# Kernel optimization log

Hardware: AMD Instinct MI355X
Metric: run time of the kernel (lower is better)

The kernel has to match this reference:

```python
import jax, jax.numpy as jnp
import numpy as np

N, E, D, D_OUT = 100000, 3200000, 64, 64
EPS = 1e-5


def setup_inputs() -> dict:
    key = jax.random.key(0)
    ks = jax.random.split(key, 16)
    s = 1.0 / np.sqrt(D)
    inp = {
        "x": jax.random.normal(ks[0], (N, D), dtype=jnp.float32),
        "edge_index": jax.random.randint(ks[1], (2, E), 0, N, dtype=jnp.int64),
        # layer 1: GCNConv weight/bias, fc weight/bias, BN gamma/beta
        "W1": jax.random.uniform(ks[2], (D, D), jnp.float32, -s, s),
        "b1": jnp.zeros((D,), jnp.float32),
        "fw1": jax.random.uniform(ks[3], (D, D), jnp.float32, -s, s),
        "fb1": jax.random.uniform(ks[4], (D,), jnp.float32, -s, s),
        "g1": jnp.ones((D,), jnp.float32),
        "bt1": jnp.zeros((D,), jnp.float32),
        # layer 2
        "W2": jax.random.uniform(ks[5], (D, D), jnp.float32, -s, s),
        "b2": jnp.zeros((D,), jnp.float32),
        "fw2": jax.random.uniform(ks[6], (D, D_OUT), jnp.float32, -s, s),
        "fb2": jax.random.uniform(ks[7], (D_OUT,), jnp.float32, -s, s),
        "g2": jnp.ones((D_OUT,), jnp.float32),
        "bt2": jnp.zeros((D_OUT,), jnp.float32),
    }
    return inp


def _gcn_conv(x, W, b, src, dst, dinv):
    # x' = X W, then symmetric-normalized scatter-add aggregation (self loops included)
    h = x @ W                                   # [N, D]
    msg = (dinv[src] * dinv[dst])[:, None] * h[src]  # [E+N, D]
    out = jax.ops.segment_sum(msg, dst, num_segments=N)
    return out + b


def _fc_bn_relu(x, fw, fb, g, bt):
    y = x @ fw + fb
    mu = jnp.mean(y, axis=0)
    var = jnp.mean((y - mu) ** 2, axis=0)  # biased var (torch BN training mode)
    y = (y - mu) * jax.lax.rsqrt(var + EPS) * g + bt
    return jax.nn.relu(y)


def reference(x, edge_index, W1, b1, fw1, fb1, g1, bt1, W2, b2, fw2, fb2, g2, bt2):
    loop = jnp.arange(N, dtype=edge_index.dtype)
    src = jnp.concatenate([edge_index[0], loop])  # add self loops
    dst = jnp.concatenate([edge_index[1], loop])
    deg = jax.ops.segment_sum(jnp.ones_like(dst, dtype=x.dtype), dst, num_segments=N)
    dinv = jax.lax.rsqrt(deg)  # deg >= 1 thanks to self loops

    h = _gcn_conv(x, W1, b1, src, dst, dinv)
    h = _fc_bn_relu(h, fw1, fb1, g1, bt1)
    h = _gcn_conv(h, W2, b2, src, dst, dinv)
    h = _fc_bn_relu(h, fw2, fb2, g2, bt2)
    return h
```

## Files before the change

### kernel.cpp

```cpp
#include <hip/hip_runtime.h>

#define N_NODES 100000
#define N_EDGES 3200000
#define D 64
#define EPS 1e-5f

#define BSHIFT 7
#define BNODES 128
#define NBUCK ((N_NODES + BNODES - 1) / BNODES)
#define P1_CHUNK 8192
#define NB_P1 ((N_EDGES + P1_CHUNK - 1) / P1_CHUNK)
#define SRC_MASK 0x1FFFFu
#define BCAP 4480
#define TBL_STRIDE 784

typedef __attribute__((ext_vector_type(8))) short bf16x8;
typedef __attribute__((ext_vector_type(4))) float f32x4;

__device__ __forceinline__ unsigned short f2bf(float f) {
  unsigned int u = __float_as_uint(f);
  u += 0x7FFFu + ((u >> 16) & 1u);
  return (unsigned short)(u >> 16);
}
__device__ __forceinline__ float bf2f(unsigned short h) {
  return __uint_as_float(((unsigned int)h) << 16);
}
__device__ __forceinline__ float2 bfpair(unsigned int u) {
  return make_float2(__uint_as_float(u << 16), __uint_as_float(u & 0xFFFF0000u));
}
__device__ __forceinline__ void addp(float2 a[4], uint4 u) {
  a[0] += bfpair(u.x);
  a[1] += bfpair(u.y);
  a[2] += bfpair(u.z);
  a[3] += bfpair(u.w);
}

__global__ __launch_bounds__(256) void combine_weights(
    const float* __restrict__ W1, const float* __restrict__ b1,
    const float* __restrict__ fw1, const float* __restrict__ fb1,
    const float* __restrict__ W2, const float* __restrict__ b2,
    const float* __restrict__ fw2, const float* __restrict__ fb2,
    unsigned int* __restrict__ WcB1, float* __restrict__ bc1,
    unsigned int* __restrict__ WcB2, float* __restrict__ bc2,
    float* __restrict__ stats) {
  if (blockIdx.x == 2) {
    if (threadIdx.x < 256) stats[threadIdx.x] = 0.0f;
    return;
  }
  const float* W  = blockIdx.x ? W2  : W1;
  const float* fw = blockIdx.x ? fw2 : fw1;
  const float* b  = blockIdx.x ? b2  : b1;
  const float* fb = blockIdx.x ? fb2 : fb1;
  unsigned int* WcB = blockIdx.x ? WcB2 : WcB1;
  float* bc = blockIdx.x ? bc2 : bc1;

  __shared__ float sW[64 * 64];
  __shared__ float sf[64 * 64];
  __shared__ float sC[64 * 64];
  for (int i = threadIdx.x; i < 4096; i += 256) { sW[i] = W[i]; sf[i] = fw[i]; }
  __syncthreads();
  for (int o = threadIdx.x; o < 4096; o += 256) {
    int i = o >> 6, j = o & 63;
    float acc = 0.f;
    #pragma unroll
    for (int k = 0; k < 64; ++k) acc += sW[i * 64 + k] * sf[k * 64 + j];
    sC[o] = acc;
  }
  __syncthreads();
  for (int o = threadIdx.x; o < 2048; o += 256) {
    int jj = o & 3, L = (o >> 2) & 63, kh = (o >> 8) & 1, nt = o >> 9;
    int k0 = (L >> 4) * 8 + jj * 2 + kh * 32;
    int n  = nt * 16 + (L & 15);
    unsigned int lo = f2bf(sC[k0 * 64 + n]);
    unsigned int hi = f2bf(sC[(k0 + 1) * 64 + n]);
    WcB[o] = (hi << 16) | lo;
  }
  if (threadIdx.x < 64) {
    int j = threadIdx.x;
    float acc = fb[j];
    #pragma unroll
    for (int k = 0; k < 64; ++k) acc += b[k] * sf[k * 64 + j];
    bc[j] = acc;
  }
}

__global__ __launch_bounds__(512) void pass1_sort(
    const int* __restrict__ src, const int* __restrict__ dst,
    unsigned int* __restrict__ stage, unsigned short* __restrict__ tbl) {
  __shared__ unsigned int hist[NBUCK];
  __shared__ unsigned int ts[512];
  __shared__ unsigned int sorted[P1_CHUNK];
  const int tid = threadIdx.x;
  const int e0 = blockIdx.x * P1_CHUNK;

  for (int b = tid; b < NBUCK; b += 512) hist[b] = 0;
  __syncthreads();

  int dreg[16];
  #pragma unroll
  for (int k = 0; k < 16; ++k) {
    int e = e0 + k * 512 + tid;
    int d = (e < N_EDGES) ? dst[e] : -1;
    dreg[k] = d;
    if (d >= 0) atomicAdd(&hist[((unsigned)d) >> BSHIFT], 1u);
  }
  __syncthreads();

  unsigned int v0 = (2 * tid < NBUCK) ? hist[2 * tid] : 0u;
  unsigned int v1 = (2 * tid + 1 < NBUCK) ? hist[2 * tid + 1] : 0u;
  unsigned int run = v0 + v1;
  ts[tid] = run;
  __syncthreads();
  for (int o = 1; o < 512; o <<= 1) {
    unsigned int add = (tid >= o) ? ts[tid - o] : 0u;
    __syncthreads();
    ts[tid] += add;
    __syncthreads();
  }
  const unsigned int excl = ts[tid] - run;
  const unsigned int m = ts[511];
  unsigned short* trow = tbl + (size_t)blockIdx.x * TBL_STRIDE;
  if (2 * tid < NBUCK)     { hist[2 * tid]     = excl;      trow[2 * tid]     = (unsigned short)excl; }
  if (2 * tid + 1 < NBUCK) { hist[2 * tid + 1] = excl + v0; trow[2 * tid + 1] = (unsigned short)(excl + v0); }
  if (tid == 0) trow[NBUCK] = (unsigned short)m;
  __syncthreads();

  #pragma unroll
  for (int k = 0; k < 16; ++k) {
    int e = e0 + k * 512 + tid;
    int t = dreg[k];
    if (t >= 0) {
      unsigned int pos = atomicAdd(&hist[((unsigned)t) >> BSHIFT], 1u);
      sorted[pos] = (((unsigned)(t & (BNODES - 1))) << 17) | (unsigned)src[e];
    }
  }
  __syncthreads();

  unsigned int* so = stage + (size_t)blockIdx.x * P1_CHUNK;
  for (int i = tid; i < (int)m; i += 512) so[i] = sorted[i];
}

__global__ __launch_bounds__(512) void pass2_sort(
    const unsigned int* __restrict__ stage, const unsigned short* __restrict__ tbl,
    int* __restrict__ eSrc, int* __restrict__ off, int* __restrict__ edeg,
    float* __restrict__ dinv, const float* __restrict__ x,
    unsigned short* __restrict__ Xs) {
  __shared__ int segbase[NB_P1];
  __shared__ int spre[512];
  __shared__ int cnt[BNODES];
  __shared__ int ts[BNODES];
  __shared__ float dinvL[BNODES];
  __shared__ unsigned int raw[BCAP];
  __shared__ int sorted[BCAP];
  const int b = blockIdx.x, tid = threadIdx.x;
  const int n0 = b * BNODES;

  int len = 0;
  if (tid < NB_P1) {
    const unsigned short* trow = tbl + (size_t)tid * TBL_STRIDE;
    int o0 = trow[b], o1 = trow[b + 1];
    segbase[tid] = tid * P1_CHUNK + o0;
    len = o1 - o0;
  }
  if (tid < BNODES) cnt[tid] = 0;
  spre[tid] = len;
  __syncthreads();
  for (int o = 1; o < 512; o <<= 1) {
    int add = (tid >= o) ? spre[tid - o] : 0;
    __syncthreads();
    spre[tid] += add;
    __syncthreads();
  }
  const int m = spre[511];
  const int pref = spre[tid] - len;

  if (tid < NB_P1) {
    const int base = segbase[tid];
    for (int j = 0; j < len; ++j) {
      unsigned int p = stage[base + j];
      raw[pref + j] = p;
      atomicAdd(&cnt[p >> 17], 1);
    }
  }
  __syncthreads();

  int v = 0;
  if (tid < BNODES) { v = cnt[tid]; ts[tid] = v; }
  __syncthreads();
  for (int o = 1; o < BNODES; o <<= 1) {
    int add = (tid >= o && tid < BNODES) ? ts[tid - o] : 0;
    __syncthreads();
    if (tid < BNODES) ts[tid] += add;
    __syncthreads();
  }
  if (tid < BNODES) {
    int excl = ts[tid] - v;
    int node = n0 + tid;
    float dv = rsqrtf((float)v + 1.0f);
    dinvL[tid] = dv;
    if (node < N_NODES) {
      off[node]  = b * BCAP + excl;
      edeg[node] = v;
      dinv[node] = dv;
    }
    cnt[tid] = excl;
  }
  __syncthreads();

  for (int i = tid; i < m; i += 512) {
    unsigned int p = raw[i];
    int pos = atomicAdd(&cnt[p >> 17], 1);
    if (pos < BCAP) sorted[pos] = (int)(p & SRC_MASK);
  }
  __syncthreads();

  int* out = eSrc + (size_t)b * BCAP;
  for (int i = tid; i < m; i += 512) out[i] = sorted[i];

  const int rows = min(BNODES, N_NODES - n0);
  for (int i = tid; i < rows * 64; i += 512) {
    int r = i >> 6;
    size_t g = (size_t)(n0 + r) * 64 + (i & 63);
    Xs[g] = f2bf(dinvL[r] * x[g]);
  }
}

__global__ __launch_bounds__(256) void agg_csr(
    const int* __restrict__ off, const int* __restrict__ edeg,
    const int* __restrict__ eSrc, const unsigned short* __restrict__ Xs,
    const float* __restrict__ dinv, unsigned short* __restrict__ agg) {
  const int wid = (blockIdx.x * 256 + threadIdx.x) >> 6;
  const int lane = threadIdx.x & 63;
  const int grp = lane >> 3, sub = lane & 7;
  if (wid >= N_NODES) return;
  const int s0 = off[wid];
  const int s1 = s0 + edeg[wid];
  const uint4* XsV = (const uint4*)Xs;

  float2 acc[4];
  {
    uint4 u = XsV[(size_t)wid * 8 + sub];
    if (grp != 0) { u.x = 0; u.y = 0; u.z = 0; u.w = 0; }
    acc[0] = bfpair(u.x);
    acc[1] = bfpair(u.y);
    acc[2] = bfpair(u.z);
    acc[3] = bfpair(u.w);
  }

  int e = s0;
  const int eend = s1 - ((s1 - s0) & 31);
  for (; e < eend; e += 32) {
    int sa = eSrc[e + grp];
    int sb = eSrc[e + 8 + grp];
    int sc = eSrc[e + 16 + grp];
    int sd = eSrc[e + 24 + grp];
    uint4 ua = XsV[(size_t)sa * 8 + sub];
    uint4 ub = XsV[(size_t)sb * 8 + sub];
    uint4 uc = XsV[(size_t)sc * 8 + sub];
    uint4 ud = XsV[(size_t)sd * 8 + sub];
    addp(acc, ua); addp(acc, ub); addp(acc, uc); addp(acc, ud);
  }
  if (e < s1) {
    const int lim = s1 - 1;
    int ea = e + grp, eb = e + 8 + grp, ec = e + 16 + grp, ed = e + 24 + grp;
    int sa = eSrc[min(ea, lim)];
    int sb = eSrc[min(eb, lim)];
    int sc = eSrc[min(ec, lim)];
    int sd = eSrc[min(ed, lim)];
    uint4 ua = XsV[(size_t)sa * 8 + sub];
    uint4 ub = XsV[(size_t)sb * 8 + sub];
    uint4 uc = XsV[(size_t)sc * 8 + sub];
    uint4 ud = XsV[(size_t)sd * 8 + sub];
    if (ea > lim) { ua.x = 0; ua.y = 0; ua.z = 0; ua.w = 0; }
    if (eb > lim) { ub.x = 0; ub.y = 0; ub.z = 0; ub.w = 0; }
    if (ec > lim) { uc.x = 0; uc.y = 0; uc.z = 0; uc.w = 0; }
    if (ed > lim) { ud.x = 0; ud.y = 0; ud.z = 0; ud.w = 0; }
    addp(acc, ua); addp(acc, ub); addp(acc, uc); addp(acc, ud);
  }

  #pragma unroll
  for (int mk = 8; mk <= 32; mk <<= 1) {
    #pragma unroll
    for (int i = 0; i < 4; ++i) {
      acc[i].x += __shfl_xor(acc[i].x, mk, 64);
      acc[i].y += __shfl_xor(acc[i].y, mk, 64);
    }
  }

  if (grp == 0) {
    float dt = dinv[wid];
    uint4 o;
    o.x = ((unsigned)f2bf(acc[0].y * dt) << 16) | f2bf(acc[0].x * dt);
    o.y = ((unsigned)f2bf(acc[1].y * dt) << 16) | f2bf(acc[1].x * dt);
    o.z = ((unsigned)f2bf(acc[2].y * dt) << 16) | f2bf(acc[2].x * dt);
    o.w = ((unsigned)f2bf(acc[3].y * dt) << 16) | f2bf(acc[3].x * dt);
    *(uint4*)(agg + (size_t)wid * 64 + sub * 8) = o;
  }
}

__global__ __launch_bounds__(256) void gemm_stats(
    const unsigned short* __restrict__ A, const unsigned int* __restrict__ WcB,
    const float* __restrict__ bc, unsigned short* __restrict__ Yb,
    float* __restrict__ colsum, float* __restrict__ colsq) {
  const int tid = threadIdx.x;
  const int L = tid & 63, wv = tid >> 6;
  const int quad = L >> 4, l16 = L & 15;

  const bf16x8* Wv = (const bf16x8*)WcB;
  bf16x8 bfr[4][2];
  #pragma unroll
  for (int nt = 0; nt < 4; ++nt)
    #pragma unroll
    for (int kh = 0; kh < 2; ++kh)
      bfr[nt][kh] = Wv[(nt * 2 + kh) * 64 + L];
  float bcv[4];
  #pragma unroll
  for (int nt = 0; nt < 4; ++nt) bcv[nt] = bc[nt * 16 + l16];

  const bf16x8* Av = (const bf16x8*)A;
  float psum[4] = {0.f, 0.f, 0.f, 0.f}, psq[4] = {0.f, 0.f, 0.f, 0.f};

  #pragma unroll
  for (int loop = 0; loop < 2; ++loop) {
    const int rowbase = blockIdx.x * 128 + loop * 64 + wv * 16;
    const int m = min(rowbase + l16, N_NODES - 1);
    bf16x8 a0 = Av[(size_t)m * 8 + quad];
    bf16x8 a1 = Av[(size_t)m * 8 + 4 + quad];
    #pragma unroll
    for (int nt = 0; nt < 4; ++nt) {
      f32x4 acc = {0.f, 0.f, 0.f, 0.f};
      acc = __builtin_amdgcn_mfma_f32_16x16x32_bf16(a0, bfr[nt][0], acc, 0, 0, 0);
      acc = __builtin_amdgcn_mfma_f32_16x16x32_bf16(a1, bfr[nt][1], acc, 0, 0, 0);
      #pragma unroll
      for (int r = 0; r < 4; ++r) {
        int row = rowbase + quad * 4 + r;
        if (row < N_NODES) {
          float y = acc[r] + bcv[nt];
          Yb[(size_t)row * 64 + nt * 16 + l16] = f2bf(y);
          psum[nt] += y;
          psq[nt] += y * y;
        }
      }
    }
  }

  #pragma unroll
  for (int nt = 0; nt < 4; ++nt) {
    psum[nt] += __shfl_xor(psum[nt], 16, 64);
    psum[nt] += __shfl_xor(psum[nt], 32, 64);
    psq[nt]  += __shfl_xor(psq[nt], 16, 64);
    psq[nt]  += __shfl_xor(psq[nt], 32, 64);
  }
  __shared__ float rsum[4][64];
  __shared__ float rsq[4][64];
  if (L < 16) {
    #pragma unroll
    for (int nt = 0; nt < 4; ++nt) {
      rsum[wv][nt * 16 + L] = psum[nt];
      rsq[wv][nt * 16 + L]  = psq[nt];
    }
  }
  __syncthreads();
  if (tid < 64) {
    float s = rsum[0][tid] + rsum[1][tid] + rsum[2][tid] + rsum[3][tid];
    float q = rsq[0][tid] + rsq[1][tid] + rsq[2][tid] + rsq[3][tid];
    atomicAdd(&colsum[tid], s);
    atomicAdd(&colsq[tid], q);
  }
}

__global__ __launch_bounds__(256) void prescale_y(
    unsigned short* __restrict__ YbXs, const float* __restrict__ dinv,
    const float* __restrict__ colsum, const float* __restrict__ colsq,
    const float* __restrict__ g, const float* __restrict__ bt) {
  __shared__ float sa[64], sc[64];
  if (threadIdx.x < 64) {
    int j = threadIdx.x;
    float mu = colsum[j] * (1.0f / N_NODES);
    float var = colsq[j] * (1.0f / N_NODES) - mu * mu;
    float s = rsqrtf(var + EPS) * g[j];
    sa[j] = s;
    sc[j] = bt[j] - mu * s;
  }
  __syncthreads();
  int idx = blockIdx.x * blockDim.x + threadIdx.x;
  if (idx < N_NODES * D) {
    int i = idx >> 6, j = idx & 63;
    float y = bf2f(YbXs[idx]);
    YbXs[idx] = f2bf(dinv[i] * fmaxf(fmaf(y, sa[j], sc[j]), 0.f));
  }
}

__global__ __launch_bounds__(256) void final_norm(
    const unsigned short* __restrict__ Yb, float* __restrict__ out,
    const float* __restrict__ colsum, const float* __restrict__ colsq,
    const float* __restrict__ g, const float* __restrict__ bt) {
  __shared__ float sa[64], sc[64];
  if (threadIdx.x < 64) {
    int j = threadIdx.x;
    float mu = colsum[j] * (1.0f / N_NODES);
    float var = colsq[j] * (1.0f / N_NODES) - mu * mu;
    float s = rsqrtf(var + EPS) * g[j];
    sa[j] = s;
    sc[j] = bt[j] - mu * s;
  }
  __syncthreads();
  int idx = blockIdx.x * blockDim.x + threadIdx.x;
  if (idx < N_NODES * D) {
    int j = idx & 63;
    out[idx] = fmaxf(fmaf(bf2f(Yb[idx]), sa[j], sc[j]), 0.f);
  }
}

extern "C" void kernel_launch(void* const* d_in, const int* in_sizes, int n_in,
                              void* d_out, int out_size, void* d_ws, size_t ws_size,
                              hipStream_t stream) {
  const float* x   = (const float*)d_in[0];
  const int*   src = (const int*)d_in[1];
  const int*   dst = src + N_EDGES;
  const float* W1  = (const float*)d_in[2];
  const float* b1  = (const float*)d_in[3];
  const float* fw1 = (const float*)d_in[4];
  const float* fb1 = (const float*)d_in[5];
  const float* g1  = (const float*)d_in[6];
  const float* bt1 = (const float*)d_in[7];
  const float* W2  = (const float*)d_in[8];
  const float* b2  = (const float*)d_in[9];
  const float* fw2 = (const float*)d_in[10];
  const float* fb2 = (const float*)d_in[11];
  const float* g2  = (const float*)d_in[12];
  const float* bt2 = (const float*)d_in[13];

  float* out = (float*)d_out;

  unsigned char* w = (unsigned char*)d_ws;
  unsigned int*   stage = (unsigned int*)w;
  unsigned short* aggb  = (unsigned short*)w;
  size_t ofs = ((size_t)NB_P1 * P1_CHUNK * 4 + 255) & ~(size_t)255;
  float*          dinv  = (float*)(w + ofs);
  unsigned short* XsYb  = (unsigned short*)(dinv + N_NODES);
  int*            eSrc  = (int*)(XsYb + (size_t)N_NODES * D);
  int*            off   = eSrc + (size_t)NBUCK * BCAP;
  int*            edeg  = off + N_NODES;
  unsigned short* tbl   = (unsigned short*)(edeg + N_NODES);
  unsigned int* WcB1 = (unsigned int*)(tbl + (size_t)NB_P1 * TBL_STRIDE);
  float* bc1  = (float*)(WcB1 + 2048);
  unsigned int* WcB2 = (unsigned int*)(bc1 + 64);
  float* bc2  = (float*)(WcB2 + 2048);
  float* sum1 = bc2 + 64;
  float* sq1  = sum1 + 64;
  float* sum2 = sq1 + 64;
  float* sq2  = sum2 + 64;

  const int nd = N_NODES * D;
  dim3 blk(256);

  combine_weights<<<3, blk, 0, stream>>>(W1, b1, fw1, fb1, W2, b2, fw2, fb2,
                                         WcB1, bc1, WcB2, bc2, sum1);

  pass1_sort<<<NB_P1, 512, 0, stream>>>(src, dst, stage, tbl);
  pass2_sort<<<NBUCK, 512, 0, stream>>>(stage, tbl, eSrc, off, edeg, dinv, x, XsYb);

  agg_csr<<<(nd + 255) / 256, blk, 0, stream>>>(off, edeg, eSrc, XsYb, dinv, aggb);
  gemm_stats<<<(N_NODES + 127) / 128, blk, 0, stream>>>(aggb, WcB1, bc1, XsYb, sum1, sq1);

  prescale_y<<<(nd + 255) / 256, blk, 0, stream>>>(XsYb, dinv, sum1, sq1, g1, bt1);
  agg_csr<<<(nd + 255) / 256, blk, 0, stream>>>(off, edeg, eSrc, XsYb, dinv, aggb);
  gemm_stats<<<(N_NODES + 127) / 128, blk, 0, stream>>>(aggb, WcB2, bc2, XsYb, sum2, sq2);

  final_norm<<<(nd + 255) / 256, blk, 0, stream>>>(XsYb, out, sum2, sq2, g2, bt2);
}
```

Measured before the change: 354.6 us.

## Assign 8 nodes per wave in CSR aggregation with padded neighbor lists

The aggregation kernel moves from one wavefront per node, which used a cross-lane shuffle reduction, to eight nodes per wavefront with eight lanes per node. Each node's neighbor list is padded to a multiple of four with a sentinel index that points to an all-zero row, so the indices can be read as int4. Loop bounds use a per-wave max count, which removes the tail handling and the shuffles. The cost is wasted loads for padding and divergence when the eight nodes in a wave have different degrees, plus a larger eSrc buffer.

```diff
diff --git a/kernel.cpp b/kernel.cpp
--- a/kernel.cpp
+++ b/kernel.cpp
@@ -11,8 +11,11 @@
 #define P1_CHUNK 8192
 #define NB_P1 ((N_EDGES + P1_CHUNK - 1) / P1_CHUNK)
 #define SRC_MASK 0x1FFFFu
-#define BCAP 4480
+#define RAWCAP 4480
+#define BCAP 5120
 #define TBL_STRIDE 784
+#define SENT N_NODES
+#define NWAVE (N_NODES / 8)
 
 typedef __attribute__((ext_vector_type(8))) short bf16x8;
 typedef __attribute__((ext_vector_type(4))) float f32x4;
@@ -42,9 +45,10 @@
     const float* __restrict__ fw2, const float* __restrict__ fb2,
     unsigned int* __restrict__ WcB1, float* __restrict__ bc1,
     unsigned int* __restrict__ WcB2, float* __restrict__ bc2,
-    float* __restrict__ stats) {
+    float* __restrict__ stats, unsigned short* __restrict__ Xs) {
   if (blockIdx.x == 2) {
     if (threadIdx.x < 256) stats[threadIdx.x] = 0.0f;
+    if (threadIdx.x < 64) Xs[(size_t)N_NODES * D + threadIdx.x] = 0;
     return;
   }
   const float* W  = blockIdx.x ? W2  : W1;
@@ -142,15 +146,16 @@
 
 __global__ __launch_bounds__(512) void pass2_sort(
     const unsigned int* __restrict__ stage, const unsigned short* __restrict__ tbl,
-    int* __restrict__ eSrc, int* __restrict__ off, int* __restrict__ edeg,
-    float* __restrict__ dinv, const float* __restrict__ x,
-    unsigned short* __restrict__ Xs) {
+    int* __restrict__ eSrc, int* __restrict__ off, int* __restrict__ pq,
+    int* __restrict__ wmax, float* __restrict__ dinv,
+    const float* __restrict__ x, unsigned short* __restrict__ Xs) {
   __shared__ int segbase[NB_P1];
   __shared__ int spre[512];
   __shared__ int cnt[BNODES];
+  __shared__ int pqs[BNODES];
   __shared__ int ts[BNODES];
   __shared__ float dinvL[BNODES];
-  __shared__ unsigned int raw[BCAP];
+  __shared__ unsigned int raw[RAWCAP];
   __shared__ int sorted[BCAP];
   const int b = blockIdx.x, tid = threadIdx.x;
   const int n0 = b * BNODES;
@@ -184,8 +189,8 @@
   }
   __syncthreads();
 
-  int v = 0;
-  if (tid < BNODES) { v = cnt[tid]; ts[tid] = v; }
+  int v = 0, pc = 0;
+  if (tid < BNODES) { v = cnt[tid]; pc = (v + 3) & ~3; ts[tid] = pc; }
   __syncthreads();
   for (int o = 1; o < BNODES; o <<= 1) {
     int add = (tid >= o && tid < BNODES) ? ts[tid - o] : 0;
@@ -193,29 +198,40 @@
     if (tid < BNODES) ts[tid] += add;
     __syncthreads();
   }
+  const int mp = ts[BNODES - 1];
   if (tid < BNODES) {
-    int excl = ts[tid] - v;
+    int excl = ts[tid] - pc;
     int node = n0 + tid;
     float dv = rsqrtf((float)v + 1.0f);
     dinvL[tid] = dv;
+    pqs[tid] = pc >> 2;
     if (node < N_NODES) {
-      off[node]  = b * BCAP + excl;
-      edeg[node] = v;
+      off[node] = b * BCAP + excl;
+      pq[node]  = pc >> 2;
       dinv[node] = dv;
     }
     cnt[tid] = excl;
   }
   __syncthreads();
+  if (tid < BNODES / 8) {
+    int mx = 0;
+    #pragma unroll
+    for (int k = 0; k < 8; ++k) mx = max(mx, pqs[tid * 8 + k]);
+    int n8 = n0 + tid * 8;
+    if (n8 < N_NODES) wmax[n8 >> 3] = mx;
+  }
+  for (int i = tid; i < mp; i += 512) sorted[i] = SENT;
+  __syncthreads();
 
   for (int i = tid; i < m; i += 512) {
     unsigned int p = raw[i];
     int pos = atomicAdd(&cnt[p >> 17], 1);
-    if (pos < BCAP) sorted[pos] = (int)(p & SRC_MASK);
+    sorted[pos] = (int)(p & SRC_MASK);
   }
   __syncthreads();
 
   int* out = eSrc + (size_t)b * BCAP;
-  for (int i = tid; i < m; i += 512) out[i] = sorted[i];
+  for (int i = tid; i < mp; i += 512) out[i] = sorted[i];
 
   const int rows = min(BNODES, N_NODES - n0);
   for (int i = tid; i < rows * 64; i += 512) {
@@ -226,76 +242,45 @@
 }
 
 __global__ __launch_bounds__(256) void agg_csr(
-    const int* __restrict__ off, const int* __restrict__ edeg,
-    const int* __restrict__ eSrc, const unsigned short* __restrict__ Xs,
-    const float* __restrict__ dinv, unsigned short* __restrict__ agg) {
+    const int* __restrict__ off, const int* __restrict__ pq,
+    const int* __restrict__ wmax, const int* __restrict__ eSrc,
+    const unsigned short* __restrict__ Xs, const float* __restrict__ dinv,
+    unsigned short* __restrict__ agg) {
   const int wid = (blockIdx.x * 256 + threadIdx.x) >> 6;
   const int lane = threadIdx.x & 63;
-  const int grp = lane >> 3, sub = lane & 7;
-  if (wid >= N_NODES) return;
-  const int s0 = off[wid];
-  const int s1 = s0 + edeg[wid];
+  const int g = lane >> 3, sub = lane & 7;
+  const int n = wid * 8 + g;
   const uint4* XsV = (const uint4*)Xs;
 
+  const int o = off[n];
+  const int q = pq[n];
+  const int wq = wmax[wid];
+  const float dv = dinv[n];
+
+  uint4 u0 = XsV[(size_t)n * 8 + sub];
   float2 acc[4];
-  {
-    uint4 u = XsV[(size_t)wid * 8 + sub];
-    if (grp != 0) { u.x = 0; u.y = 0; u.z = 0; u.w = 0; }
-    acc[0] = bfpair(u.x);
-    acc[1] = bfpair(u.y);
-    acc[2] = bfpair(u.z);
-    acc[3] = bfpair(u.w);
-  }
-
-  int e = s0;
-  const int eend = s1 - ((s1 - s0) & 31);
-  for (; e < eend; e += 32) {
-    int sa = eSrc[e + grp];
-    int sb = eSrc[e + 8 + grp];
-    int sc = eSrc[e + 16 + grp];
-    int sd = eSrc[e + 24 + grp];
-    uint4 ua = XsV[(size_t)sa * 8 + sub];
-    uint4 ub = XsV[(size_t)sb * 8 + sub];
-    uint4 uc = XsV[(size_t)sc * 8 + sub];
-    uint4 ud = XsV[(size_t)sd * 8 + sub];
+  acc[0] = bfpair(u0.x);
+  acc[1] = bfpair(u0.y);
+  acc[2] = bfpair(u0.z);
+  acc[3] = bfpair(u0.w);
+
+  const int4* E = (const int4*)(eSrc + o);
+  for (int it = 0; it < wq; ++it) {
+    int4 idx = E[it];
+    if (it >= q) { idx.x = SENT; idx.y = SENT; idx.z = SENT; idx.w = SENT; }
+    uint4 ua = XsV[(size_t)idx.x * 8 + sub];
+    uint4 ub = XsV[(size_t)idx.y * 8 + sub];
+    uint4 uc = XsV[(size_t)idx.z * 8 + sub];
+    uint4 ud = XsV[(size_t)idx.w * 8 + sub];
     addp(acc, ua); addp(acc, ub); addp(acc, uc); addp(acc, ud);
   }
-  if (e < s1) {
-    const int lim = s1 - 1;
-    int ea = e + grp, eb = e + 8 + grp, ec = e + 16 + grp, ed = e + 24 + grp;
-    int sa = eSrc[min(ea, lim)];
-    int sb = eSrc[min(eb, lim)];
-    int sc = eSrc[min(ec, lim)];
-    int sd = eSrc[min(ed, lim)];
-    uint4 ua = XsV[(size_t)sa * 8 + sub];
-    uint4 ub = XsV[(size_t)sb * 8 + sub];
-    uint4 uc = XsV[(size_t)sc * 8 + sub];
-    uint4 ud = XsV[(size_t)sd * 8 + sub];
-    if (ea > lim) { ua.x = 0; ua.y = 0; ua.z = 0; ua.w = 0; }
-    if (eb > lim) { ub.x = 0; ub.y = 0; ub.z = 0; ub.w = 0; }
-    if (ec > lim) { uc.x = 0; uc.y = 0; uc.z = 0; uc.w = 0; }
-    if (ed > lim) { ud.x = 0; ud.y = 0; ud.z = 0; ud.w = 0; }
-    addp(acc, ua); addp(acc, ub); addp(acc, uc); addp(acc, ud);
-  }
-
-  #pragma unroll
-  for (int mk = 8; mk <= 32; mk <<= 1) {
-    #pragma unroll
-    for (int i = 0; i < 4; ++i) {
-      acc[i].x += __shfl_xor(acc[i].x, mk, 64);
-      acc[i].y += __shfl_xor(acc[i].y, mk, 64);
-    }
-  }
-
-  if (grp == 0) {
-    float dt = dinv[wid];
-    uint4 o;
-    o.x = ((unsigned)f2bf(acc[0].y * dt) << 16) | f2bf(acc[0].x * dt);
-    o.y = ((unsigned)f2bf(acc[1].y * dt) << 16) | f2bf(acc[1].x * dt);
-    o.z = ((unsigned)f2bf(acc[2].y * dt) << 16) | f2bf(acc[2].x * dt);
-    o.w = ((unsigned)f2bf(acc[3].y * dt) << 16) | f2bf(acc[3].x * dt);
-    *(uint4*)(agg + (size_t)wid * 64 + sub * 8) = o;
-  }
+
+  uint4 o4;
+  o4.x = ((unsigned)f2bf(acc[0].y * dv) << 16) | f2bf(acc[0].x * dv);
+  o4.y = ((unsigned)f2bf(acc[1].y * dv) << 16) | f2bf(acc[1].x * dv);
+  o4.z = ((unsigned)f2bf(acc[2].y * dv) << 16) | f2bf(acc[2].x * dv);
+  o4.w = ((unsigned)f2bf(acc[3].y * dv) << 16) | f2bf(acc[3].x * dv);
+  *(uint4*)(agg + (size_t)n * 64 + sub * 8) = o4;
 }
 
 __global__ __launch_bounds__(256) void gemm_stats(
@@ -439,10 +424,11 @@
   size_t ofs = ((size_t)NB_P1 * P1_CHUNK * 4 + 255) & ~(size_t)255;
   float*          dinv  = (float*)(w + ofs);
   unsigned short* XsYb  = (unsigned short*)(dinv + N_NODES);
-  int*            eSrc  = (int*)(XsYb + (size_t)N_NODES * D);
-  int*            off   = eSrc + (size_t)NBUCK * BCAP;
-  int*            edeg  = off + N_NODES;
-  unsigned short* tbl   = (unsigned short*)(edeg + N_NODES);
+  int*            eSrc  = (int*)(XsYb + (size_t)(N_NODES + 8) * D);
+  int*            off   = eSrc + (size_t)NBUCK * BCAP + 1024;
+  int*            pq    = off + N_NODES;
+  int*            wmax  = pq + N_NODES;
+  unsigned short* tbl   = (unsigned short*)(wmax + NWAVE);
   unsigned int* WcB1 = (unsigned int*)(tbl + (size_t)NB_P1 * TBL_STRIDE);
   float* bc1  = (float*)(WcB1 + 2048);
   unsigned int* WcB2 = (unsigned int*)(bc1 + 64);
@@ -456,16 +442,16 @@
   dim3 blk(256);
 
   combine_weights<<<3, blk, 0, stream>>>(W1, b1, fw1, fb1, W2, b2, fw2, fb2,
-                                         WcB1, bc1, WcB2, bc2, sum1);
+                                         WcB1, bc1, WcB2, bc2, sum1, XsYb);
 
   pass1_sort<<<NB_P1, 512, 0, stream>>>(src, dst, stage, tbl);
-  pass2_sort<<<NBUCK, 512, 0, stream>>>(stage, tbl, eSrc, off, edeg, dinv, x, XsYb);
-
-  agg_csr<<<(nd + 255) / 256, blk, 0, stream>>>(off, edeg, eSrc, XsYb, dinv, aggb);
+  pass2_sort<<<NBUCK, 512, 0, stream>>>(stage, tbl, eSrc, off, pq, wmax, dinv, x, XsYb);
+
+  agg_csr<<<NWAVE / 4, blk, 0, stream>>>(off, pq, wmax, eSrc, XsYb, dinv, aggb);
   gemm_stats<<<(N_NODES + 127) / 128, blk, 0, stream>>>(aggb, WcB1, bc1, XsYb, sum1, sq1);
 
   prescale_y<<<(nd + 255) / 256, blk, 0, stream>>>(XsYb, dinv, sum1, sq1, g1, bt1);
-  agg_csr<<<(nd + 255) / 256, blk, 0, stream>>>(off, edeg, eSrc, XsYb, dinv, aggb);
+  agg_csr<<<NWAVE / 4, blk, 0, stream>>>(off, pq, wmax, eSrc, XsYb, dinv, aggb);
   gemm_stats<<<(N_NODES + 127) / 128, blk, 0, stream>>>(aggb, WcB2, bc2, XsYb, sum2, sq2);
 
   final_norm<<<(nd + 255) / 256, blk, 0, stream>>>(XsYb, out, sum2, sq2, g2, bt2);
```

Result: slower. 365.2 us (+3.0%).
